# Kernel tuning notes

Hardware: AMD Instinct MI355X
Metric: run time of the kernel (lower is better)

Reference implementation:

```python
import jax, jax.numpy as jnp
import numpy as np

N_HEADS = 8
HEAD_C = 48
NC = N_HEADS * HEAD_C  # 384
N_GROUPS = 4
GC = NC // N_GROUPS  # 96
STRIDE = 2
EPS = 1e-5


def conv1x1(x, w, b):
    # x: (B,C,H,W), w: (O,C), b: (O,)
    return jnp.einsum('bchw,oc->bohw', x, w) + b[None, :, None, None]


def ref_points(Hk, Wk, dtype):
    ry = jnp.linspace(0.5, Hk - 0.5, Hk, dtype=dtype) / (Hk - 1.0) * 2.0 - 1.0
    rx = jnp.linspace(0.5, Wk - 0.5, Wk, dtype=dtype) / (Wk - 1.0) * 2.0 - 1.0
    return jnp.stack(jnp.meshgrid(ry, rx, indexing='ij'), axis=-1)  # (Hk,Wk,2) in (y,x)


def grid_sample_bilinear(img, grid):
    # img: (N,C,H,W); grid: (N,Hg,Wg,2) xy in [-1,1]; align_corners=True, zeros padding
    N, C, H, W = img.shape
    gx = (grid[..., 0] + 1.0) * 0.5 * (W - 1)
    gy = (grid[..., 1] + 1.0) * 0.5 * (H - 1)
    x0 = jnp.floor(gx); y0 = jnp.floor(gy)
    x1 = x0 + 1.0;      y1 = y0 + 1.0
    wx1 = gx - x0; wx0 = 1.0 - wx1
    wy1 = gy - y0; wy0 = 1.0 - wy1

    def gather(ix, iy):
        valid = (ix >= 0) & (ix <= W - 1) & (iy >= 0) & (iy <= H - 1)
        ixc = jnp.clip(ix, 0, W - 1).astype(jnp.int32)
        iyc = jnp.clip(iy, 0, H - 1).astype(jnp.int32)
        vals = jax.vmap(lambda im, yy, xx: im[:, yy, xx])(img, iyc, ixc)  # (N,C,Hg,Wg)
        return vals * valid[:, None].astype(img.dtype)

    v00 = gather(x0, y0); v01 = gather(x1, y0)
    v10 = gather(x0, y1); v11 = gather(x1, y1)
    return (v00 * (wx0 * wy0)[:, None] + v01 * (wx1 * wy0)[:, None]
            + v10 * (wx0 * wy1)[:, None] + v11 * (wx1 * wy1)[:, None])


def _forward(x, Wq, bq, Wk, bk, Wv, bv, Wo, bo,
             off_dw_w, off_dw_b, ln_g, ln_b, off_pw_w):
    B, C, H, W = x.shape
    q = conv1x1(x, Wq, bq)                               # (B,C,H,W)
    q_off = q.reshape(B * N_GROUPS, GC, H, W)
    # offset net: depthwise 3x3 stride-2 conv -> channel LN -> GELU -> 1x1 to 2 ch
    h = jax.lax.conv_general_dilated(
        q_off, off_dw_w, (STRIDE, STRIDE), ((1, 1), (1, 1)),
        dimension_numbers=('NCHW', 'OIHW', 'NCHW'), feature_group_count=GC)
    h = h + off_dw_b[None, :, None, None]
    mu = h.mean(axis=1, keepdims=True)
    var = ((h - mu) ** 2).mean(axis=1, keepdims=True)
    h = (h - mu) / jnp.sqrt(var + EPS) * ln_g[None, :, None, None] + ln_b[None, :, None, None]
    h = jax.nn.gelu(h, approximate=False)
    offset = jnp.einsum('bchw,oc->bohw', h, off_pw_w)    # (B*g, 2, Hk, Wk), ch0=y, ch1=x
    Hk, Wk_ = offset.shape[2], offset.shape[3]
    rng = jnp.array([1.0 / (Hk - 1.0), 1.0 / (Wk_ - 1.0)], x.dtype).reshape(1, 2, 1, 1)
    offset = jnp.tanh(offset) * rng                      # offset_range_factor = 1
    offset = offset.transpose(0, 2, 3, 1)                # (B*g, Hk, Wk, 2) yx
    ref = ref_points(Hk, Wk_, x.dtype)                   # (Hk, Wk, 2) yx
    pos = offset + ref[None]
    xs = grid_sample_bilinear(x.reshape(B * N_GROUPS, GC, H, W), pos[..., ::-1])
    n = Hk * Wk_
    xs = xs.reshape(B, C, 1, n)
    k = conv1x1(xs, Wk, bk).reshape(B * N_HEADS, HEAD_C, n)
    v = conv1x1(xs, Wv, bv).reshape(B * N_HEADS, HEAD_C, n)
    qh = q.reshape(B * N_HEADS, HEAD_C, H * W)
    attn = jnp.einsum('bcm,bcn->bmn', qh, k) * (HEAD_C ** -0.5)
    attn = jax.nn.softmax(attn, axis=2)
    out = jnp.einsum('bmn,bcn->bcm', attn, v).reshape(B, C, H, W)
    y = conv1x1(out, Wo, bo)
    ref_b = jnp.broadcast_to(ref[None, None], (B, N_GROUPS, Hk, Wk_, 2))
    return y, pos.reshape(B, N_GROUPS, Hk, Wk_, 2), ref_b


def setup_inputs() -> dict:
    key = jax.random.key(0)
    ks = jax.random.split(key, 12)
    s = 0.02
    return {
        'x': jax.random.normal(ks[0], (8, NC, 56, 56), jnp.float32),
        'Wq': jax.random.normal(ks[1], (NC, NC), jnp.float32) * s,
        'bq': jnp.zeros((NC,), jnp.float32),
        'Wk': jax.random.normal(ks[2], (NC, NC), jnp.float32) * s,
        'bk': jnp.zeros((NC,), jnp.float32),
        'Wv': jax.random.normal(ks[3], (NC, NC), jnp.float32) * s,
        'bv': jnp.zeros((NC,), jnp.float32),
        'Wo': jax.random.normal(ks[4], (NC, NC), jnp.float32) * s,
        'bo': jnp.zeros((NC,), jnp.float32),
        'off_dw_w': jax.random.normal(ks[5], (GC, 1, 3, 3), jnp.float32) * 0.1,
        'off_dw_b': jnp.zeros((GC,), jnp.float32),
        'ln_g': jnp.ones((GC,), jnp.float32),
        'ln_b': jnp.zeros((GC,), jnp.float32),
        'off_pw_w': jax.random.normal(ks[6], (2, GC), jnp.float32) * 0.1,
    }


def reference(x, Wq, bq, Wk, bk, Wv, bv, Wo, bo,
              off_dw_w, off_dw_b, ln_g, ln_b, off_pw_w):
    return _forward(x, Wq, bq, Wk, bk, Wv, bv, Wo, bo,
                    off_dw_w, off_dw_b, ln_g, ln_b, off_pw_w)
```

## Files before the change

kernel.cpp:

```cpp
#include <hip/hip_runtime.h>
#include <math.h>

constexpr int BATCH = 8;
constexpr int NC    = 384;
constexpr int H     = 56, W = 56, HW = 3136;
constexpr int NPTS  = 784;
constexpr int NG    = 4, GC = 96;
constexpr int NH    = 8, HC = 48;

typedef __attribute__((ext_vector_type(8))) short short8;
typedef __attribute__((ext_vector_type(4))) float f32x4;
typedef __attribute__((ext_vector_type(4))) unsigned short us4;

__device__ inline unsigned short f2bf(float f) {
    union { float f; unsigned u; } v; v.f = f;
    unsigned r = v.u + 0x7FFF + ((v.u >> 16) & 1);
    return (unsigned short)(r >> 16);
}
__device__ inline unsigned short f2bf_t(float f) {
    union { float f; unsigned u; } v; v.f = f;
    return (unsigned short)(v.u >> 16);
}
__device__ inline float bf2f(unsigned short u) {
    union { unsigned u; float f; } v; v.u = (unsigned)u << 16;
    return v.f;
}
__device__ inline float wred_sum(float v) {
    #pragma unroll
    for (int off = 32; off > 0; off >>= 1) v += __shfl_xor(v, off);
    return v;
}

__global__ __launch_bounds__(256) void transpose_cvt(
    const float* __restrict__ x, unsigned short* __restrict__ xT)
{
    __shared__ unsigned short Ls[64 * 68];
    int b = blockIdx.z, c0 = blockIdx.y * 64, hw0 = blockIdx.x * 64;
    const float* xb = x + ((size_t)b * NC + c0) * HW + hw0;
    int t = threadIdx.x;
    #pragma unroll
    for (int i = 0; i < 4; i++) {
        int u = t + i * 256;
        int cc = u >> 4, f4 = (u & 15) * 4;
        float4 v = *(const float4*)&xb[(size_t)cc * HW + f4];
        us4 p; p[0] = f2bf(v.x); p[1] = f2bf(v.y); p[2] = f2bf(v.z); p[3] = f2bf(v.w);
        *(us4*)&Ls[cc * 68 + f4] = p;
    }
    __syncthreads();
    unsigned short* xTb = xT + ((size_t)b * HW + hw0) * NC + c0;
    #pragma unroll
    for (int i = 0; i < 4; i++) {
        int u = t + i * 256;
        int hw = u >> 4, cg = (u & 15) * 4;
        us4 p;
        p[0] = Ls[(cg + 0) * 68 + hw];
        p[1] = Ls[(cg + 1) * 68 + hw];
        p[2] = Ls[(cg + 2) * 68 + hw];
        p[3] = Ls[(cg + 3) * 68 + hw];
        *(us4*)&xTb[(size_t)hw * NC + cg] = p;
    }
}

__global__ __launch_bounds__(256) void wcvt(
    const float* __restrict__ w0, const float* __restrict__ w1,
    const float* __restrict__ w2, const float* __restrict__ w3,
    unsigned short* __restrict__ o0, unsigned short* __restrict__ okv,
    unsigned short* __restrict__ o3)
{
    const float* src; unsigned short* dst;
    switch (blockIdx.y) {
        case 0: src = w0; dst = o0; break;
        case 1: src = w1; dst = okv; break;
        case 2: src = w2; dst = okv + NC * NC; break;
        default: src = w3; dst = o3; break;
    }
    int idx = (blockIdx.x * 256 + threadIdx.x) * 4;
    float4 v = *(const float4*)&src[idx];
    us4 p; p[0] = f2bf(v.x); p[1] = f2bf(v.y); p[2] = f2bf(v.z); p[3] = f2bf(v.w);
    *(us4*)&dst[idx] = p;
}

template<int MODE>
__global__ __launch_bounds__(256) void gemm_bf16(
    const unsigned short* __restrict__ A, const float* __restrict__ bias,
    const float* __restrict__ bias2, const unsigned short* __restrict__ BT,
    float* __restrict__ Cf, unsigned short* __restrict__ Cb,
    unsigned short* __restrict__ Cb2, int N)
{
    int b  = blockIdx.z;
    int n0 = blockIdx.x * 128;
    int m0 = blockIdx.y * 128;
    const unsigned short* BTb = BT + (size_t)b * N * NC;

    __shared__ unsigned short As[128 * 40];
    __shared__ unsigned short Bs[128 * 40];

    int t = threadIdx.x;
    int wave = t >> 6, lane = t & 63;
    int quad = lane >> 4, col = lane & 15;
    int wm = (wave >> 1) * 64, wn = (wave & 1) * 64;

    const short8 z8 = {0,0,0,0,0,0,0,0};
    f32x4 acc[4][4];
    #pragma unroll
    for (int i = 0; i < 4; i++)
        #pragma unroll
        for (int j = 0; j < 4; j++) acc[i][j] = (f32x4){0.f, 0.f, 0.f, 0.f};

    for (int k0 = 0; k0 < NC; k0 += 32) {
        #pragma unroll
        for (int i = 0; i < 2; i++) {
            int u = t + i * 256;
            int mm = u >> 2, kc = (u & 3) * 8;
            *(short8*)&As[mm * 40 + kc] =
                *(const short8*)&A[(size_t)(m0 + mm) * NC + k0 + kc];
        }
        #pragma unroll
        for (int i = 0; i < 2; i++) {
            int u = t + i * 256;
            int nn = u >> 2, kc = (u & 3) * 8;
            short8 val = z8;
            if (n0 + nn < N)
                val = *(const short8*)&BTb[(size_t)(n0 + nn) * NC + k0 + kc];
            *(short8*)&Bs[nn * 40 + kc] = val;
        }
        __syncthreads();

        short8 af[4], bf[4];
        #pragma unroll
        for (int mt = 0; mt < 4; mt++)
            af[mt] = *(const short8*)&As[(wm + mt * 16 + col) * 40 + quad * 8];
        #pragma unroll
        for (int nt = 0; nt < 4; nt++)
            bf[nt] = *(const short8*)&Bs[(wn + nt * 16 + col) * 40 + quad * 8];
        #pragma unroll
        for (int mt = 0; mt < 4; mt++)
            #pragma unroll
            for (int nt = 0; nt < 4; nt++)
                acc[mt][nt] = __builtin_amdgcn_mfma_f32_16x16x32_bf16(
                    af[mt], bf[nt], acc[mt][nt], 0, 0, 0);
        __syncthreads();
    }

    if constexpr (MODE == 0) {
        float* Cfb = Cf + (size_t)b * NC * N;
        #pragma unroll
        for (int mt = 0; mt < 4; mt++) {
            #pragma unroll
            for (int r = 0; r < 4; r++) {
                int m = m0 + wm + mt * 16 + quad * 4 + r;
                float bv = bias[m];
                #pragma unroll
                for (int nt = 0; nt < 4; nt++) {
                    int n = n0 + wn + nt * 16 + col;
                    if (n < N) Cfb[(size_t)m * N + n] = acc[mt][nt][r] + bv;
                }
            }
        }
    } else if constexpr (MODE == 2) {
        unsigned short* Kb = Cb + (size_t)b * N * NC;
        #pragma unroll
        for (int mt = 0; mt < 4; mt++) {
            int mb = m0 + wm + mt * 16 + quad * 4;
            float bv[4];
            #pragma unroll
            for (int r = 0; r < 4; r++) bv[r] = bias[mb + r];
            #pragma unroll
            for (int nt = 0; nt < 4; nt++) {
                int n = n0 + wn + nt * 16 + col;
                if (n < N) {
                    us4 p;
                    #pragma unroll
                    for (int r = 0; r < 4; r++) p[r] = f2bf(acc[mt][nt][r] + bv[r]);
                    *(us4*)&Kb[(size_t)n * NC + mb] = p;
                }
            }
        }
    } else {
        if (m0 < NC) {
            unsigned short* Kb = Cb + (size_t)b * N * NC;
            #pragma unroll
            for (int mt = 0; mt < 4; mt++) {
                int mb = m0 + wm + mt * 16 + quad * 4;
                float bv[4];
                #pragma unroll
                for (int r = 0; r < 4; r++) bv[r] = bias[mb + r];
                #pragma unroll
                for (int nt = 0; nt < 4; nt++) {
                    int n = n0 + wn + nt * 16 + col;
                    if (n < N) {
                        us4 p;
                        #pragma unroll
                        for (int r = 0; r < 4; r++) p[r] = f2bf(acc[mt][nt][r] + bv[r]);
                        *(us4*)&Kb[(size_t)n * NC + mb] = p;
                    }
                }
            }
        } else {
            unsigned short* Vb = Cb2 + (size_t)b * NC * N;
            #pragma unroll
            for (int mt = 0; mt < 4; mt++) {
                #pragma unroll
                for (int r = 0; r < 4; r++) {
                    int m = m0 - NC + wm + mt * 16 + quad * 4 + r;
                    float bv = bias2[m];
                    #pragma unroll
                    for (int nt = 0; nt < 4; nt++) {
                        int n = n0 + wn + nt * 16 + col;
                        if (n < N) Vb[(size_t)m * N + n] = f2bf(acc[mt][nt][r] + bv);
                    }
                }
            }
        }
    }
}

__global__ __launch_bounds__(256) void offset_kernel(
    const unsigned short* __restrict__ qT, const float* __restrict__ dww,
    const float* __restrict__ dwb, const float* __restrict__ lng,
    const float* __restrict__ lnb, const float* __restrict__ pww,
    float* __restrict__ pos_out,   float* __restrict__ ref_out)
{
    int wave = threadIdx.x >> 6, l = threadIdx.x & 63;
    int bg = blockIdx.y, b = bg >> 2, g = bg & 3;
    int s  = blockIdx.x * 4 + wave;
    int py = s / 28, px = s - py * 28;
    bool has2 = l < 32;
    int c0 = l, c1 = 64 + l;

    const unsigned short* qb = qT + (size_t)b * HW * NC + g * GC;

    float h0 = 0.f, h1 = 0.f;
    #pragma unroll
    for (int ky = 0; ky < 3; ky++) {
        int yy = py * 2 - 1 + ky;
        if (yy < 0 || yy >= H) continue;
        #pragma unroll
        for (int kx = 0; kx < 3; kx++) {
            int xx = px * 2 - 1 + kx;
            if (xx < 0 || xx >= W) continue;
            const unsigned short* row = qb + (size_t)(yy * W + xx) * NC;
            float w0 = dww[c0 * 9 + ky * 3 + kx];
            h0 = fmaf(bf2f(row[c0]), w0, h0);
            if (has2) {
                float w1 = dww[c1 * 9 + ky * 3 + kx];
                h1 = fmaf(bf2f(row[c1]), w1, h1);
            }
        }
    }
    h0 += dwb[c0];
    if (has2) h1 += dwb[c1];

    float mu = wred_sum(h0 + (has2 ? h1 : 0.f)) * (1.f / GC);
    float d0 = h0 - mu, d1 = h1 - mu;
    float var = wred_sum(d0 * d0 + (has2 ? d1 * d1 : 0.f)) * (1.f / GC);
    float rstd = rsqrtf(var + 1e-5f);

    float hn0 = d0 * rstd * lng[c0] + lnb[c0];
    float ge0 = 0.5f * hn0 * (1.f + erff(hn0 * 0.70710678118654752f));
    float ge1 = 0.f;
    if (has2) {
        float hn1 = d1 * rstd * lng[c1] + lnb[c1];
        ge1 = 0.5f * hn1 * (1.f + erff(hn1 * 0.70710678118654752f));
    }

    float offy = wred_sum(ge0 * pww[c0] + (has2 ? ge1 * pww[c1] : 0.f));
    float offx = wred_sum(ge0 * pww[GC + c0] + (has2 ? ge1 * pww[GC + c1] : 0.f));

    if (l == 0) {
        float ry = (2.f * py + 1.f) / 27.f - 1.f;
        float rx = (2.f * px + 1.f) / 27.f - 1.f;
        size_t idx = ((size_t)bg * NPTS + s) * 2;
        pos_out[idx]     = tanhf(offy) * (1.f / 27.f) + ry;
        pos_out[idx + 1] = tanhf(offx) * (1.f / 27.f) + rx;
        ref_out[idx]     = ry;
        ref_out[idx + 1] = rx;
    }
}

__global__ __launch_bounds__(256) void sample_kernel(
    const unsigned short* __restrict__ xT, const float* __restrict__ pos,
    unsigned short* __restrict__ xsT)
{
    int bg = blockIdx.y;
    int b  = bg >> 2, g = bg & 3;
    int s  = blockIdx.x * 8 + (threadIdx.x >> 5);
    int l  = threadIdx.x & 31;

    const float* pg = pos + ((size_t)bg * NPTS + s) * 2;
    float py = pg[0], px = pg[1];
    float gx = (px + 1.f) * 27.5f;
    float gy = (py + 1.f) * 27.5f;
    float x0f = floorf(gx), y0f = floorf(gy);
    int ix0 = (int)x0f, iy0 = (int)y0f;
    int ix1 = ix0 + 1,  iy1 = iy0 + 1;
    float wx1 = gx - x0f, wx0 = 1.f - wx1;
    float wy1 = gy - y0f, wy0 = 1.f - wy1;
    bool vx0 = (ix0 >= 0) && (ix0 < W);
    bool vx1 = (ix1 >= 0) && (ix1 < W);
    bool vy0 = (iy0 >= 0) && (iy0 < H);
    bool vy1 = (iy1 >= 0) && (iy1 < H);
    int cx0 = vx0 ? ix0 : 0, cx1 = vx1 ? ix1 : 0;
    int cy0 = vy0 ? iy0 : 0, cy1 = vy1 ? iy1 : 0;
    float w00 = (vx0 && vy0) ? wx0 * wy0 : 0.f;
    float w01 = (vx1 && vy0) ? wx1 * wy0 : 0.f;
    float w10 = (vx0 && vy1) ? wx0 * wy1 : 0.f;
    float w11 = (vx1 && vy1) ? wx1 * wy1 : 0.f;

    const unsigned short* xb = xT + (size_t)b * HW * NC + g * GC;
    const unsigned short* r00 = xb + (size_t)(cy0 * W + cx0) * NC;
    const unsigned short* r01 = xb + (size_t)(cy0 * W + cx1) * NC;
    const unsigned short* r10 = xb + (size_t)(cy1 * W + cx0) * NC;
    const unsigned short* r11 = xb + (size_t)(cy1 * W + cx1) * NC;
    unsigned short* orow = xsT + ((size_t)b * NPTS + s) * NC + g * GC;
    #pragma unroll
    for (int ci = 0; ci < 3; ci++) {
        int c = l + ci * 32;
        float val = bf2f(r00[c]) * w00 + bf2f(r01[c]) * w01
                  + bf2f(r10[c]) * w10 + bf2f(r11[c]) * w11;
        orow[c] = f2bf(val);
    }
}

#define PS_STRIDE 40

__device__ inline short8 scale8(short8 v, float s) {
    short8 r;
    #pragma unroll
    for (int j = 0; j < 8; j++)
        r[j] = (short)f2bf(bf2f((unsigned short)v[j]) * s);
    return r;
}

__global__ __launch_bounds__(256) void attn_mfma(
    const unsigned short* __restrict__ qT, const unsigned short* __restrict__ kt,
    const unsigned short* __restrict__ vt, unsigned short* __restrict__ aoT)
{
    __shared__ __align__(16) unsigned short Ps[8 * 16 * PS_STRIDE];

    int t    = threadIdx.x;
    int wave = t >> 6, lane = t & 63;
    int quad = lane >> 4, col = lane & 15;

    int bh = blockIdx.y;
    int b  = bh >> 3, h = bh & 7;
    int m0 = blockIdx.x * 128;
    const unsigned short* KT = kt + (size_t)b * NPTS * NC + h * HC;
    const unsigned short* VT = vt + ((size_t)b * NC + h * HC) * NPTS;

    const float scale = 0.14433756729740643f;
    const short8 z8 = {0,0,0,0,0,0,0,0};

    int gm0 = m0 + wave * 32 + col;
    int gm1 = gm0 + 16;
    short8 qb0[2], qb1[2];
    {
        int cg0 = gm0 < HW ? gm0 : HW - 1;
        int cg1 = gm1 < HW ? gm1 : HW - 1;
        const unsigned short* r0 = qT + ((size_t)b * HW + cg0) * NC + h * HC;
        const unsigned short* r1 = qT + ((size_t)b * HW + cg1) * NC + h * HC;
        qb0[0] = scale8(*(const short8*)&r0[quad * 8], scale);
        qb0[1] = scale8(*(const short8*)&r1[quad * 8], scale);
        if (quad < 2) {
            qb1[0] = scale8(*(const short8*)&r0[32 + quad * 8], scale);
            qb1[1] = scale8(*(const short8*)&r1[32 + quad * 8], scale);
        } else { qb1[0] = z8; qb1[1] = z8; }
    }

    unsigned short* pane0 = Ps + (wave * 2 + 0) * 16 * PS_STRIDE;
    unsigned short* pane1 = Ps + (wave * 2 + 1) * 16 * PS_STRIDE;

    float l_acc[2] = {0.f, 0.f};
    f32x4 acc_o[2][3];
    #pragma unroll
    for (int s2 = 0; s2 < 2; s2++)
        #pragma unroll
        for (int ct = 0; ct < 3; ct++) acc_o[s2][ct] = (f32x4){0.f, 0.f, 0.f, 0.f};

    for (int ci = 0; ci < 7; ci++) {
        int k0 = ci * 128;

        #pragma unroll
        for (int s2 = 0; s2 < 4; s2++) {
            #pragma unroll
            for (int jth = 0; jth < 2; jth++) {
                int jt = s2 * 2 + jth;
                int key = k0 + jt * 16 + col;
                key = key < NPTS ? key : NPTS - 1;
                const unsigned short* krow = KT + (size_t)key * NC;
                short8 kb0 = *(const short8*)&krow[quad * 8];
                short8 kb1 = (quad < 2) ? *(const short8*)&krow[32 + quad * 8] : z8;
                bool valid = (k0 + jt * 16) < NPTS;
                #pragma unroll
                for (int set = 0; set < 2; set++) {
                    f32x4 sa = {0.f, 0.f, 0.f, 0.f};
                    sa = __builtin_amdgcn_mfma_f32_16x16x32_bf16(kb0, qb0[set], sa, 0, 0, 0);
                    sa = __builtin_amdgcn_mfma_f32_16x16x32_bf16(kb1, qb1[set], sa, 0, 0, 0);
                    us4 p = {0, 0, 0, 0};
                    if (valid) {
                        #pragma unroll
                        for (int r = 0; r < 4; r++) {
                            float pv = __expf(sa[r]);
                            l_acc[set] += pv;
                            p[r] = f2bf_t(pv);
                        }
                    }
                    unsigned short* pane = set ? pane1 : pane0;
                    *(us4*)&pane[col * PS_STRIDE + jth * 16 + quad * 4] = p;
                }
            }
            short8 pb0 = *(const short8*)&pane0[col * PS_STRIDE + quad * 8];
            short8 pb1 = *(const short8*)&pane1[col * PS_STRIDE + quad * 8];
            int voff = k0 + s2 * 32 + quad * 8;
            voff = voff <= (NPTS - 8) ? voff : (NPTS - 8);
            #pragma unroll
            for (int ct = 0; ct < 3; ct++) {
                short8 va = *(const short8*)&VT[(size_t)(ct * 16 + col) * NPTS + voff];
                acc_o[0][ct] = __builtin_amdgcn_mfma_f32_16x16x32_bf16(va, pb0, acc_o[0][ct], 0, 0, 0);
                acc_o[1][ct] = __builtin_amdgcn_mfma_f32_16x16x32_bf16(va, pb1, acc_o[1][ct], 0, 0, 0);
            }
        }
    }

    #pragma unroll
    for (int set = 0; set < 2; set++) {
        float l = l_acc[set];
        l += __shfl_xor(l, 16);
        l += __shfl_xor(l, 32);
        float inv = 1.f / l;
        int gm = set ? gm1 : gm0;
        if (gm < HW) {
            unsigned short* orow = aoT + ((size_t)b * HW + gm) * NC + h * HC;
            #pragma unroll
            for (int ct = 0; ct < 3; ct++) {
                us4 p;
                #pragma unroll
                for (int r = 0; r < 4; r++) p[r] = f2bf(acc_o[set][ct][r] * inv);
                *(us4*)&orow[ct * 16 + quad * 4] = p;
            }
        }
    }
}

extern "C" void kernel_launch(void* const* d_in, const int* in_sizes, int n_in,
                              void* d_out, int out_size, void* d_ws, size_t ws_size,
                              hipStream_t stream)
{
    const float* x   = (const float*)d_in[0];
    const float* Wq  = (const float*)d_in[1];
    const float* bq  = (const float*)d_in[2];
    const float* Wk  = (const float*)d_in[3];
    const float* bk  = (const float*)d_in[4];
    const float* Wv  = (const float*)d_in[5];
    const float* bv  = (const float*)d_in[6];
    const float* Wo  = (const float*)d_in[7];
    const float* bo  = (const float*)d_in[8];
    const float* dww = (const float*)d_in[9];
    const float* dwb = (const float*)d_in[10];
    const float* lng = (const float*)d_in[11];
    const float* lnb = (const float*)d_in[12];
    const float* pww = (const float*)d_in[13];

    float* out     = (float*)d_out;
    float* y_out   = out;
    float* pos_out = out + (size_t)BATCH * NC * HW;
    float* ref_out = pos_out + (size_t)BATCH * NG * NPTS * 2;

    const size_t NBIG = (size_t)BATCH * NC * HW;
    const size_t NSML = (size_t)BATCH * NC * NPTS;

    unsigned short* xT   = (unsigned short*)d_ws;
    unsigned short* qT   = xT   + NBIG;
    unsigned short* xsT  = qT   + NBIG;
    unsigned short* kt_w = xsT  + NSML;
    unsigned short* vt_w = kt_w + NSML;
    unsigned short* aoT  = vt_w + NSML;
    unsigned short* wqb  = aoT  + NBIG;
    unsigned short* wob  = wqb + NC * NC;
    unsigned short* wkv  = wob + NC * NC;

    transpose_cvt<<<dim3(49, 6, BATCH), 256, 0, stream>>>(x, xT);
    wcvt<<<dim3(144, 4), 256, 0, stream>>>(Wq, Wk, Wv, Wo, wqb, wkv, wob);
    gemm_bf16<2><<<dim3(25, 3, BATCH), 256, 0, stream>>>(
        wqb, bq, nullptr, xT, nullptr, qT, nullptr, HW);
    offset_kernel<<<dim3(196, BATCH * NG), 256, 0, stream>>>(
        qT, dww, dwb, lng, lnb, pww, pos_out, ref_out);
    sample_kernel<<<dim3(98, BATCH * NG), 256, 0, stream>>>(xT, pos_out, xsT);
    gemm_bf16<4><<<dim3(7, 6, BATCH), 256, 0, stream>>>(
        wkv, bk, bv, xsT, nullptr, kt_w, vt_w, NPTS);
    attn_mfma<<<dim3((HW + 127) / 128, BATCH * NH), 256, 0, stream>>>(
        qT, kt_w, vt_w, aoT);
    gemm_bf16<0><<<dim3(25, 3, BATCH), 256, 0, stream>>>(
        wob, bo, nullptr, aoT, y_out, nullptr, nullptr, HW);
}
```

Baseline: 331.2 us.

## Stage K/V tiles in shared memory with register prefetch, double queries per block

The attention kernel now cooperatively loads each 128-key chunk of K and V into LDS once per block, and prefetches the next chunk into registers while computing the current one. Before, each wave read its K and V fragments directly from global memory. Each block now handles 256 queries instead of 128, with four query sets per wave, so every staged K/V tile is reused across more queries. The cost is more registers and LDS per block, two barriers per chunk, and about half as many blocks, which lowers occupancy and parallelism and adds tail waste on the last query tile.

```diff
diff --git a/kernel.cpp b/kernel.cpp
--- a/kernel.cpp
+++ b/kernel.cpp
@@ -322,6 +322,8 @@
     }
 }
 
+#define KS_STRIDE 56
+#define VS_STRIDE 136
 #define PS_STRIDE 40
 
 __device__ inline short8 scale8(short8 v, float s) {
@@ -336,7 +338,10 @@
     const unsigned short* __restrict__ qT, const unsigned short* __restrict__ kt,
     const unsigned short* __restrict__ vt, unsigned short* __restrict__ aoT)
 {
-    __shared__ __align__(16) unsigned short Ps[8 * 16 * PS_STRIDE];
+    __shared__ __align__(16) unsigned short smem[23936];
+    unsigned short* Ks = smem;
+    unsigned short* Vs = Ks + 128 * KS_STRIDE;
+    unsigned short* Ps = Vs + 48 * VS_STRIDE;
 
     int t    = threadIdx.x;
     int wave = t >> 6, lane = t & 63;
@@ -344,55 +349,92 @@
 
     int bh = blockIdx.y;
     int b  = bh >> 3, h = bh & 7;
-    int m0 = blockIdx.x * 128;
+    int m0 = blockIdx.x * 256;
     const unsigned short* KT = kt + (size_t)b * NPTS * NC + h * HC;
     const unsigned short* VT = vt + ((size_t)b * NC + h * HC) * NPTS;
 
     const float scale = 0.14433756729740643f;
     const short8 z8 = {0,0,0,0,0,0,0,0};
 
-    int gm0 = m0 + wave * 32 + col;
-    int gm1 = gm0 + 16;
-    short8 qb0[2], qb1[2];
+    int gmq[4];
+    short8 qb0[4], qb1[4];
+    #pragma unroll
+    for (int set = 0; set < 4; set++) {
+        int gm = m0 + wave * 64 + set * 16 + col;
+        gmq[set] = gm;
+        int cg = gm < HW ? gm : HW - 1;
+        const unsigned short* r0 = qT + ((size_t)b * HW + cg) * NC + h * HC;
+        qb0[set] = scale8(*(const short8*)&r0[quad * 8], scale);
+        qb1[set] = (quad < 2) ? scale8(*(const short8*)&r0[32 + quad * 8], scale) : z8;
+    }
+
+    unsigned short* paneW = Ps + wave * 4 * 16 * PS_STRIDE;
+
+    float l_acc[4] = {0.f, 0.f, 0.f, 0.f};
+    f32x4 acc_o[4][3];
+    #pragma unroll
+    for (int set = 0; set < 4; set++)
+        #pragma unroll
+        for (int ct = 0; ct < 3; ct++) acc_o[set][ct] = (f32x4){0.f, 0.f, 0.f, 0.f};
+
+    int skey  = t >> 1;
+    int spart = (t & 1) * 3;
+    short8 kreg[3], vreg[3];
+
     {
-        int cg0 = gm0 < HW ? gm0 : HW - 1;
-        int cg1 = gm1 < HW ? gm1 : HW - 1;
-        const unsigned short* r0 = qT + ((size_t)b * HW + cg0) * NC + h * HC;
-        const unsigned short* r1 = qT + ((size_t)b * HW + cg1) * NC + h * HC;
-        qb0[0] = scale8(*(const short8*)&r0[quad * 8], scale);
-        qb0[1] = scale8(*(const short8*)&r1[quad * 8], scale);
-        if (quad < 2) {
-            qb1[0] = scale8(*(const short8*)&r0[32 + quad * 8], scale);
-            qb1[1] = scale8(*(const short8*)&r1[32 + quad * 8], scale);
-        } else { qb1[0] = z8; qb1[1] = z8; }
-    }
-
-    unsigned short* pane0 = Ps + (wave * 2 + 0) * 16 * PS_STRIDE;
-    unsigned short* pane1 = Ps + (wave * 2 + 1) * 16 * PS_STRIDE;
-
-    float l_acc[2] = {0.f, 0.f};
-    f32x4 acc_o[2][3];
-    #pragma unroll
-    for (int s2 = 0; s2 < 2; s2++)
-        #pragma unroll
-        for (int ct = 0; ct < 3; ct++) acc_o[s2][ct] = (f32x4){0.f, 0.f, 0.f, 0.f};
+        bool kv = skey < NPTS;
+        const unsigned short* krow = KT + (size_t)skey * NC + spart * 8;
+        #pragma unroll
+        for (int i = 0; i < 3; i++) kreg[i] = kv ? *(const short8*)(krow + i * 8) : z8;
+        #pragma unroll
+        for (int i = 0; i < 3; i++) {
+            int li = t + i * 256;
+            int chan = li >> 4, part = li & 15;
+            vreg[i] = *(const short8*)&VT[(size_t)chan * NPTS + part * 8];
+        }
+    }
 
     for (int ci = 0; ci < 7; ci++) {
         int k0 = ci * 128;
 
         #pragma unroll
+        for (int i = 0; i < 3; i++)
+            *(short8*)&Ks[skey * KS_STRIDE + (spart + i) * 8] = kreg[i];
+        #pragma unroll
+        for (int i = 0; i < 3; i++) {
+            int li = t + i * 256;
+            int chan = li >> 4, part = li & 15;
+            *(short8*)&Vs[chan * VS_STRIDE + part * 8] = vreg[i];
+        }
+        __syncthreads();
+
+        if (ci < 6) {
+            int nk0 = k0 + 128;
+            bool kv = nk0 + skey < NPTS;
+            const unsigned short* krow = KT + (size_t)(nk0 + skey) * NC + spart * 8;
+            #pragma unroll
+            for (int i = 0; i < 3; i++) kreg[i] = kv ? *(const short8*)(krow + i * 8) : z8;
+            #pragma unroll
+            for (int i = 0; i < 3; i++) {
+                int li = t + i * 256;
+                int chan = li >> 4, part = li & 15;
+                vreg[i] = (nk0 + part * 8 < NPTS)
+                    ? *(const short8*)&VT[(size_t)chan * NPTS + nk0 + part * 8] : z8;
+            }
+        }
+
+        #pragma unroll
         for (int s2 = 0; s2 < 4; s2++) {
             #pragma unroll
             for (int jth = 0; jth < 2; jth++) {
                 int jt = s2 * 2 + jth;
-                int key = k0 + jt * 16 + col;
-                key = key < NPTS ? key : NPTS - 1;
-                const unsigned short* krow = KT + (size_t)key * NC;
-                short8 kb0 = *(const short8*)&krow[quad * 8];
-                short8 kb1 = (quad < 2) ? *(const short8*)&krow[32 + quad * 8] : z8;
+                int keyl = jt * 16 + col;
+                short8 kb0 = *(const short8*)&Ks[keyl * KS_STRIDE + quad * 8];
+                short8 kb1 = (quad < 2)
+                    ? *(const short8*)&Ks[keyl * KS_STRIDE + 32 + quad * 8] : z8;
                 bool valid = (k0 + jt * 16) < NPTS;
                 #pragma unroll
-                for (int set = 0; set < 2; set++) {
+                for (int set = 0; set < 4; set++) {
                     f32x4 sa = {0.f, 0.f, 0.f, 0.f};
                     sa = __builtin_amdgcn_mfma_f32_16x16x32_bf16(kb0, qb0[set], sa, 0, 0, 0);
                     sa = __builtin_amdgcn_mfma_f32_16x16x32_bf16(kb1, qb1[set], sa, 0, 0, 0);
@@ -405,30 +447,32 @@
                             p[r] = f2bf_t(pv);
                         }
                     }
-                    unsigned short* pane = set ? pane1 : pane0;
-                    *(us4*)&pane[col * PS_STRIDE + jth * 16 + quad * 4] = p;
+                    *(us4*)&paneW[set * 16 * PS_STRIDE + col * PS_STRIDE + jth * 16 + quad * 4] = p;
                 }
             }
-            short8 pb0 = *(const short8*)&pane0[col * PS_STRIDE + quad * 8];
-            short8 pb1 = *(const short8*)&pane1[col * PS_STRIDE + quad * 8];
-            int voff = k0 + s2 * 32 + quad * 8;
-            voff = voff <= (NPTS - 8) ? voff : (NPTS - 8);
+            short8 pb[4];
+            #pragma unroll
+            for (int set = 0; set < 4; set++)
+                pb[set] = *(const short8*)&paneW[set * 16 * PS_STRIDE + col * PS_STRIDE + quad * 8];
             #pragma unroll
             for (int ct = 0; ct < 3; ct++) {
-                short8 va = *(const short8*)&VT[(size_t)(ct * 16 + col) * NPTS + voff];
-                acc_o[0][ct] = __builtin_amdgcn_mfma_f32_16x16x32_bf16(va, pb0, acc_o[0][ct], 0, 0, 0);
-                acc_o[1][ct] = __builtin_amdgcn_mfma_f32_16x16x32_bf16(va, pb1, acc_o[1][ct], 0, 0, 0);
-            }
-        }
-    }
-
-    #pragma unroll
-    for (int set = 0; set < 2; set++) {
+                short8 va = *(const short8*)&Vs[(ct * 16 + col) * VS_STRIDE + s2 * 32 + quad * 8];
+                #pragma unroll
+                for (int set = 0; set < 4; set++)
+                    acc_o[set][ct] = __builtin_amdgcn_mfma_f32_16x16x32_bf16(
+                        va, pb[set], acc_o[set][ct], 0, 0, 0);
+            }
+        }
+        __syncthreads();
+    }
+
+    #pragma unroll
+    for (int set = 0; set < 4; set++) {
         float l = l_acc[set];
         l += __shfl_xor(l, 16);
         l += __shfl_xor(l, 32);
         float inv = 1.f / l;
-        int gm = set ? gm1 : gm0;
+        int gm = gmq[set];
         if (gm < HW) {
             unsigned short* orow = aoT + ((size_t)b * HW + gm) * NC + h * HC;
             #pragma unroll
@@ -488,7 +532,7 @@
     sample_kernel<<<dim3(98, BATCH * NG), 256, 0, stream>>>(xT, pos_out, xsT);
     gemm_bf16<4><<<dim3(7, 6, BATCH), 256, 0, stream>>>(
         wkv, bk, bv, xsT, nullptr, kt_w, vt_w, NPTS);
-    attn_mfma<<<dim3((HW + 127) / 128, BATCH * NH), 256, 0, stream>>>(
+    attn_mfma<<<dim3((HW + 255) / 256, BATCH * NH), 256, 0, stream>>>(
         qT, kt_w, vt_w, aoT);
     gemm_bf16<0><<<dim3(25, 3, BATCH), 256, 0, stream>>>(
         wob, bo, nullptr, aoT, y_out, nullptr, nullptr, HW);
```

Result: no change. 324.9 us (-1.9%).
